# Performance work log

Measured on AMD Instinct MI355X. Metric: run time of the kernel, lower is better.

The kernel has to match this reference:

```python
import jax, jax.numpy as jnp
import numpy as np

B, T, D, K = 16, 4096, 512, 256
ALPHA_MIN = 1e-6


def setup_inputs() -> dict:
    key = jax.random.key(0)
    ks = jax.random.split(key, 5)
    x = jax.random.normal(ks[0], (B, T, D), dtype=jnp.float32)
    # s_imag ~ U(-pi, pi) as in reset_parameters
    s_imag = jax.random.uniform(ks[1], (K,), minval=-np.pi, maxval=np.pi, dtype=jnp.float32)
    # s_real_raw = softplus^{-1}(target_alpha - alpha_min), target_alpha ~ U(0.01, 0.2)
    target_alpha = jax.random.uniform(ks[2], (K,), minval=0.01, maxval=0.2, dtype=jnp.float32)
    y = jnp.clip(target_alpha - ALPHA_MIN, 1e-8, None)
    s_real_raw = jnp.log(jnp.expm1(y))
    # projection weight/bias (spectral norm applied inside reference)
    W = jax.random.normal(ks[3], (K, D), dtype=jnp.float32) / np.sqrt(D)
    b = jnp.zeros((K,), dtype=jnp.float32)
    tau_raw = jnp.zeros((), dtype=jnp.float32)
    return {"x": x, "s_real_raw": s_real_raw, "s_imag": s_imag,
            "tau_raw": tau_raw, "W": W, "b": b}


def _spectral_normalize(W):
    # one power iteration from a fixed random u (mirrors torch spectral_norm buffer,
    # n_power_iterations=1, eps=1e-7); u,v are stop-gradiented like torch buffers.
    eps = 1e-7
    u0 = jax.random.normal(jax.random.key(42), (W.shape[0],), dtype=W.dtype)
    u0 = u0 / jnp.maximum(jnp.linalg.norm(u0), eps)
    v = W.T @ u0
    v = v / jnp.maximum(jnp.linalg.norm(v), eps)
    u = W @ v
    u = u / jnp.maximum(jnp.linalg.norm(u), eps)
    u = jax.lax.stop_gradient(u)
    v = jax.lax.stop_gradient(v)
    sigma = u @ (W @ v)
    return W / sigma


def reference(x, s_real_raw, s_imag, tau_raw, W, b):
    Bx, Tx, Dx = x.shape
    k = s_imag.shape[0]
    tau = jax.nn.softplus(tau_raw) + 1e-3
    alpha0 = (jax.nn.softplus(s_real_raw) + ALPHA_MIN) * tau  # [k]
    omega0 = s_imag * tau                                     # [k]
    # dt is None path: uniform normalized time step
    dt = jnp.asarray(1.0 / max(Tx - 1, 1), dtype=x.dtype)
    rho = jnp.exp(-alpha0 * dt)   # [k], time-invariant since dt is constant
    ct = jnp.cos(omega0 * dt)     # [k]
    st = jnp.sin(omega0 * dt)     # [k]
    # spectral-normalized linear drive u_t = W_sn x_t + b  -> [B,T,k]
    u = jnp.einsum('btd,kd->btk', x, _spectral_normalize(W)) + b

    def step(carry, u_t):
        c, s = carry  # each [B,k]
        c_new = rho * (c * ct - s * st) + u_t
        s_new = rho * (c * st + s * ct)
        return (c_new, s_new), (c_new, s_new)

    z0 = (jnp.zeros((Bx, k), x.dtype), jnp.zeros((Bx, k), x.dtype))
    _, (C, S) = jax.lax.scan(step, z0, jnp.swapaxes(u, 0, 1))  # [T,B,k] each
    C = jnp.swapaxes(C, 0, 1)
    S = jnp.swapaxes(S, 0, 1)
    return jnp.concatenate([C, S], axis=2)  # [B,T,2k]
```

## Files before the change

kernel.cpp:

```cpp
#include <hip/hip_runtime.h>

#define Bsz 16
#define Tsz 4096
#define Dsz 512
#define Ksz 256
#define Msz (Bsz * Tsz)
#define CHUNK 64
#define NCH (Tsz / CHUNK)

typedef __attribute__((ext_vector_type(8))) short short8;
typedef __attribute__((ext_vector_type(4))) float f32x4;

__device__ __forceinline__ unsigned int rotl32(unsigned int x, int d) {
  return (x << d) | (x >> (32 - d));
}

__device__ void threefry_pair(unsigned int c0, unsigned int c1,
                              unsigned int& o0, unsigned int& o1) {
  const unsigned int k0 = 0u, k1 = 42u;
  const unsigned int k2 = k0 ^ k1 ^ 0x1BD11BDAu;
  unsigned int x0 = c0 + k0;
  unsigned int x1 = c1 + k1;
#define TF_ROUND(r) { x0 += x1; x1 = rotl32(x1, (r)); x1 ^= x0; }
  TF_ROUND(13) TF_ROUND(15) TF_ROUND(26) TF_ROUND(6)
  x0 += k1; x1 += k2 + 1u;
  TF_ROUND(17) TF_ROUND(29) TF_ROUND(16) TF_ROUND(24)
  x0 += k2; x1 += k0 + 2u;
  TF_ROUND(13) TF_ROUND(15) TF_ROUND(26) TF_ROUND(6)
  x0 += k0; x1 += k1 + 3u;
  TF_ROUND(17) TF_ROUND(29) TF_ROUND(16) TF_ROUND(24)
  x0 += k1; x1 += k2 + 4u;
  TF_ROUND(13) TF_ROUND(15) TF_ROUND(26) TF_ROUND(6)
  x0 += k2; x1 += k0 + 5u;
#undef TF_ROUND
  o0 = x0; o1 = x1;
}

__device__ float erfinv32(float x) {
  float w = -log1pf(-x * x);
  float p;
  if (w < 5.f) {
    w -= 2.5f;
    p = 2.81022636e-08f;
    p = fmaf(p, w, 3.43273939e-07f);
    p = fmaf(p, w, -3.5233877e-06f);
    p = fmaf(p, w, -4.39150654e-06f);
    p = fmaf(p, w, 0.00021858087f);
    p = fmaf(p, w, -0.00125372503f);
    p = fmaf(p, w, -0.00417768164f);
    p = fmaf(p, w, 0.246640727f);
    p = fmaf(p, w, 1.50140941f);
  } else {
    w = sqrtf(w) - 3.f;
    p = -0.000200214257f;
    p = fmaf(p, w, 0.000100950558f);
    p = fmaf(p, w, 0.00134934322f);
    p = fmaf(p, w, -0.00367342844f);
    p = fmaf(p, w, 0.00573950773f);
    p = fmaf(p, w, -0.0076224613f);
    p = fmaf(p, w, 0.00943887047f);
    p = fmaf(p, w, 1.00167406f);
    p = fmaf(p, w, 2.83297682f);
  }
  return p * x;
}

__device__ float bits_to_normal(unsigned int bits) {
  unsigned int fb = (bits >> 9) | 0x3f800000u;
  float f = __uint_as_float(fb) - 1.0f;
  const float lo = -0.99999994f;
  float u = f * 2.0f + lo;
  u = fmaxf(lo, u);
  return 1.41421356f * erfinv32(u);
}

__device__ float block_sum_512(float v, float* s_red) {
  #pragma unroll
  for (int o = 32; o > 0; o >>= 1) v += __shfl_down(v, o);
  const int lane = threadIdx.x & 63, wid = threadIdx.x >> 6;
  if (lane == 0) s_red[wid] = v;
  __syncthreads();
  float r = 0.f;
  #pragma unroll
  for (int i = 0; i < 8; ++i) r += s_red[i];
  __syncthreads();
  return r;
}

__device__ __forceinline__ unsigned int bf16rne(float f) {
  unsigned int u = __float_as_uint(f);
  return (u + 0x7FFFu + ((u >> 16) & 1u)) >> 16;
}

__global__ __launch_bounds__(512) void prep1_kernel(
    const float* __restrict__ W, float* __restrict__ partial_v) {
  __shared__ float s_u0[Ksz];
  __shared__ float s_red[8];
  const int tid = threadIdx.x;
  if (tid < 128) {
    unsigned int y0, y1;
    threefry_pair((unsigned int)tid, (unsigned int)(tid + 128), y0, y1);
    s_u0[tid] = bits_to_normal(y0);
    s_u0[tid + 128] = bits_to_normal(y1);
  }
  __syncthreads();
  float val = (tid < Ksz) ? s_u0[tid] * s_u0[tid] : 0.f;
  float ss = block_sum_512(val, s_red);
  float inv = 1.f / fmaxf(sqrtf(ss), 1e-7f);

  const int k0 = blockIdx.x * 16;
  float acc = 0.f;
  #pragma unroll
  for (int kk = 0; kk < 16; ++kk)
    acc = fmaf(W[(size_t)(k0 + kk) * Dsz + tid], s_u0[k0 + kk], acc);
  partial_v[blockIdx.x * Dsz + tid] = acc * inv;
}

__global__ __launch_bounds__(512) void prep2_kernel(
    const float* __restrict__ W, const float* __restrict__ partial_v,
    float* __restrict__ wv) {
  __shared__ float s_v[Dsz];
  __shared__ float s_red[8];
  __shared__ float s_p[8];
  const int tid = threadIdx.x;
  float acc = 0.f;
  #pragma unroll
  for (int b = 0; b < 16; ++b) acc += partial_v[b * Dsz + tid];
  float ssv = block_sum_512(acc * acc, s_red);
  float invv = 1.f / fmaxf(sqrtf(ssv), 1e-7f);
  s_v[tid] = acc * invv;
  __syncthreads();

  const int k = blockIdx.x * 4 + (tid >> 7);
  const int sub = tid & 127;
  const float* wr = W + (size_t)k * Dsz;
  float p = 0.f;
  #pragma unroll
  for (int j = sub; j < Dsz; j += 128) p = fmaf(wr[j], s_v[j], p);
  #pragma unroll
  for (int o = 32; o > 0; o >>= 1) p += __shfl_down(p, o);
  const int lane = tid & 63, wid = tid >> 6;
  if (lane == 0) s_p[wid] = p;
  __syncthreads();
  if (tid < 4) wv[blockIdx.x * 4 + tid] = s_p[2 * tid] + s_p[2 * tid + 1];
}

__global__ __launch_bounds__(256) void prep3_kernel(
    const float* __restrict__ s_real_raw, const float* __restrict__ s_imag,
    const float* __restrict__ tau_raw, const float* __restrict__ wv,
    float* __restrict__ consts) {
  __shared__ float s_p[4];
  const int tid = threadIdx.x;
  float v = wv[tid];
  float v2 = v * v;
  #pragma unroll
  for (int o = 32; o > 0; o >>= 1) v2 += __shfl_down(v2, o);
  const int lane = tid & 63, wid = tid >> 6;
  if (lane == 0) s_p[wid] = v2;
  __syncthreads();
  float sswv = s_p[0] + s_p[1] + s_p[2] + s_p[3];
  float sigma = sswv / fmaxf(sqrtf(sswv), 1e-7f);
  if (tid == 0) consts[12 * Ksz] = 1.f / sigma;

  float tr = tau_raw[0];
  float tau = fmaxf(tr, 0.f) + log1pf(expf(-fabsf(tr))) + 1e-3f;
  float srr = s_real_raw[tid];
  float sp = fmaxf(srr, 0.f) + log1pf(expf(-fabsf(srr)));
  float alpha0 = (sp + 1e-6f) * tau;
  float omega0 = s_imag[tid] * tau;
  const float dt = 1.f / 4095.f;
  float ad = alpha0 * dt, an = omega0 * dt;
  consts[tid]            = expf(-ad) * cosf(an);
  consts[Ksz + tid]      = expf(-ad) * sinf(an);
  consts[2 * Ksz + tid]  = expf(-ad * 64.f) * cosf(an * 64.f);
  consts[3 * Ksz + tid]  = expf(-ad * 64.f) * sinf(an * 64.f);
  consts[4 * Ksz + tid]  = expf(-ad * 4.f) * cosf(an * 4.f);
  consts[5 * Ksz + tid]  = expf(-ad * 4.f) * sinf(an * 4.f);
  consts[6 * Ksz + tid]  = expf(-ad * 8.f) * cosf(an * 8.f);
  consts[7 * Ksz + tid]  = expf(-ad * 8.f) * sinf(an * 8.f);
  consts[8 * Ksz + tid]  = expf(-ad * 16.f) * cosf(an * 16.f);
  consts[9 * Ksz + tid]  = expf(-ad * 16.f) * sinf(an * 16.f);
  consts[10 * Ksz + tid] = expf(-ad * 32.f) * cosf(an * 32.f);
  consts[11 * Ksz + tid] = expf(-ad * 32.f) * sinf(an * 32.f);
}

__global__ __launch_bounds__(64) void wpack_kernel(
    const float* __restrict__ W, const float* __restrict__ consts,
    unsigned int* __restrict__ WfH, unsigned int* __restrict__ WfL) {
  const int kb = blockIdx.x >> 4;
  const int nb = blockIdx.x & 15;
  const int lane = threadIdx.x;
  const int lr = lane & 15, lg = lane >> 4;
  const float inv_sigma = consts[12 * Ksz];
  const float* src = W + (size_t)(nb * 16 + lr) * Dsz + kb * 32 + lg * 8;
  float v[8];
  *(float4*)&v[0] = *(const float4*)src;
  *(float4*)&v[4] = *(const float4*)(src + 4);
  unsigned int hh[4], ll[4];
  #pragma unroll
  for (int i = 0; i < 4; ++i) {
    float v0 = v[2 * i] * inv_sigma, v1 = v[2 * i + 1] * inv_sigma;
    unsigned int u0 = __float_as_uint(v0);
    unsigned int u1 = __float_as_uint(v1);
    hh[i] = (u0 >> 16) | (u1 & 0xFFFF0000u);
    float r0 = v0 - __uint_as_float(u0 & 0xFFFF0000u);
    float r1 = v1 - __uint_as_float(u1 & 0xFFFF0000u);
    ll[i] = bf16rne(r0) | (bf16rne(r1) << 16);
  }
  const size_t off = (size_t)blockIdx.x * 256 + lane * 4;
  *(int4*)(WfH + off) = *(int4*)hh;
  *(int4*)(WfL + off) = *(int4*)ll;
}

__global__ __launch_bounds__(512, 2) void gemm_mfma(
    const float* __restrict__ X, const unsigned int* __restrict__ WfH,
    const unsigned int* __restrict__ WfL, const float* __restrict__ bias,
    const float* __restrict__ consts, unsigned short* __restrict__ U,
    float* __restrict__ carry) {
  __shared__ unsigned int ldsA[2][4096];

  const int tid = threadIdx.x;
  const size_t m0 = (size_t)blockIdx.x * 128;

  const int sr = tid >> 2;
  const int sc = (tid & 3) * 8;
  const float* gx = X + (m0 + sr) * Dsz + sc;
  const int swz = (sr & 7) << 4;
  const int aoff_h = sr * 128 + ((sc * 2) ^ swz);
  const int aoff_l = sr * 128 + ((64 + sc * 2) ^ swz);

  const int lane = tid & 63;
  const int wid = tid >> 6;
  const int wm = wid >> 2;
  const int wn = wid & 3;
  const int lr = lane & 15;
  const int lg = lane >> 4;

  float xaA[8], xaB[8];
  #define LOAD_A(dst, kb) do {                             \
    const float* p = gx + (kb) * 32;                       \
    *(float4*)&dst[0] = *(const float4*)p;                 \
    *(float4*)&dst[4] = *(const float4*)(p + 4);           \
  } while (0)

  const char* const wfh = (const char*)WfH + (size_t)wn * 4096 + lane * 16;
  const char* const wfl = (const char*)WfL + (size_t)wn * 4096 + lane * 16;

  short8 bhA[4], blA[4], bhB[4], blB[4];
  #define LOAD_B(bh_, bl_, kb) do {                                          \
    const size_t tb = (size_t)(kb) * 16384;                                  \
    _Pragma("unroll")                                                        \
    for (int f = 0; f < 4; ++f) {                                            \
      bh_[f] = *(const short8*)(wfh + tb + (size_t)f * 1024);                \
      bl_[f] = *(const short8*)(wfl + tb + (size_t)f * 1024);                \
    }                                                                        \
  } while (0)

  #define CONVERT_STORE(xa, buf) do {                                        \
    char* const Ab_ = (char*)ldsA[(buf)];                                    \
    unsigned int hh[4], llw[4];                                              \
    _Pragma("unroll")                                                        \
    for (int i = 0; i < 4; ++i) {                                            \
      float v0 = xa[2 * i], v1 = xa[2 * i + 1];                              \
      unsigned int u0 = __float_as_uint(v0);                                 \
      unsigned int u1 = __float_as_uint(v1);                                 \
      hh[i] = (u0 >> 16) | (u1 & 0xFFFF0000u);                               \
      float r0 = v0 - __uint_as_float(u0 & 0xFFFF0000u);                     \
      float r1 = v1 - __uint_as_float(u1 & 0xFFFF0000u);                     \
      llw[i] = bf16rne(r0) | (bf16rne(r1) << 16);                            \
    }                                                                        \
    *(int4*)(Ab_ + aoff_h) = *(int4*)hh;                                     \
    *(int4*)(Ab_ + aoff_l) = *(int4*)llw;                                    \
  } while (0)

  short8 ah[4], al[4];
  #define DS_READ(buf) do {                                                  \
    const char* const Ab_ = (const char*)ldsA[(buf)];                        \
    _Pragma("unroll")                                                        \
    for (int f = 0; f < 4; ++f) {                                            \
      const int r = wm * 64 + f * 16 + lr;                                   \
      const int sz = (r & 7) << 4;                                           \
      ah[f] = *(const short8*)(Ab_ + r * 128 + ((lg * 16) ^ sz));            \
      al[f] = *(const short8*)(Ab_ + r * 128 + ((64 + lg * 16) ^ sz));       \
    }                                                                        \
  } while (0)

  f32x4 acc[4][4];
  #pragma unroll
  for (int i = 0; i < 4; ++i)
    #pragma unroll
    for (int j = 0; j < 4; ++j) acc[i][j] = (f32x4)(0.f);

  #define MFMA48(bh_, bl_) do {                                              \
    _Pragma("unroll")                                                        \
    for (int mf = 0; mf < 4; ++mf)                                           \
      _Pragma("unroll")                                                      \
      for (int nf = 0; nf < 4; ++nf)                                         \
        acc[mf][nf] = __builtin_amdgcn_mfma_f32_16x16x32_bf16(               \
            ah[mf], bh_[nf], acc[mf][nf], 0, 0, 0);                          \
    _Pragma("unroll")                                                        \
    for (int mf = 0; mf < 4; ++mf)                                           \
      _Pragma("unroll")                                                      \
      for (int nf = 0; nf < 4; ++nf)                                         \
        acc[mf][nf] = __builtin_amdgcn_mfma_f32_16x16x32_bf16(               \
            ah[mf], bl_[nf], acc[mf][nf], 0, 0, 0);                          \
    _Pragma("unroll")                                                        \
    for (int mf = 0; mf < 4; ++mf)                                           \
      _Pragma("unroll")                                                      \
      for (int nf = 0; nf < 4; ++nf)                                         \
        acc[mf][nf] = __builtin_amdgcn_mfma_f32_16x16x32_bf16(               \
            al[mf], bh_[nf], acc[mf][nf], 0, 0, 0);                          \
  } while (0)

  #define SYNC() do {                                                        \
    asm volatile("s_waitcnt lgkmcnt(0)" ::: "memory");                       \
    __builtin_amdgcn_s_barrier();                                            \
    __builtin_amdgcn_sched_barrier(0);                                       \
  } while (0)

  LOAD_A(xaA, 0);
  LOAD_A(xaB, 1);
  LOAD_B(bhA, blA, 0);

  #define BODY(kb, xa, bhC, blC, bhN, blN) do {                              \
    char* const Ab = (char*)ldsA[(kb) & 1]; (void)Ab;                        \
    if ((kb) + 1 < 16) LOAD_B(bhN, blN, (kb) + 1);        \
    CONVERT_STORE(xa, (kb) & 1);                                             \
    if ((kb) + 2 < 16) LOAD_A(xa, (kb) + 2);                   \
    SYNC();                                                                  \
    DS_READ((kb) & 1);                                                       \
    MFMA48(bhC, blC);                                                        \
  } while (0)

  for (int kb = 0; kb < 16; kb += 2) {
    BODY(kb,     xaA, bhA, blA, bhB, blB);
    BODY(kb + 1, xaB, bhB, blB, bhA, blA);
  }
  #undef BODY
  #undef SYNC
  #undef MFMA48
  #undef DS_READ
  #undef CONVERT_STORE
  #undef LOAD_B
  #undef LOAD_A

  #pragma unroll
  for (int nf = 0; nf < 4; ++nf) {
    const int n = wn * 64 + nf * 16 + lr;
    const float bv = bias[n];
    const float ar_ = consts[n],           ai_ = consts[Ksz + n];
    const float p4r = consts[4 * Ksz + n], p4i = consts[5 * Ksz + n];
    const float p8r = consts[6 * Ksz + n], p8i = consts[7 * Ksz + n];
    const float p16r = consts[8 * Ksz + n], p16i = consts[9 * Ksz + n];
    const int e = 3 - lg;
    const float b1r = (e & 1) ? p4r : 1.f, b1i = (e & 1) ? p4i : 0.f;
    const float b2r = (e & 2) ? p8r : 1.f, b2i = (e & 2) ? p8i : 0.f;
    float wr = b1r * b2r - b1i * b2i;
    float wi = b1r * b2i + b1i * b2r;
    float Sr = 0.f, Si = 0.f;
    #pragma unroll
    for (int mf = 3; mf >= 0; --mf) {
      float vr = wr, vi = wi;
      #pragma unroll
      for (int j = 3; j >= 0; --j) {
        const float u = acc[mf][nf][j] + bv;
        U[(m0 + wm * 64 + mf * 16 + lg * 4 + j) * Ksz + n] =
            (unsigned short)bf16rne(u);
        Sr = fmaf(u, vr, Sr);
        Si = fmaf(u, vi, Si);
        if (j) {
          float t_ = vr * ar_ - vi * ai_;
          vi = vr * ai_ + vi * ar_;
          vr = t_;
        }
      }
      if (mf) {
        float t_ = wr * p16r - wi * p16i;
        wi = wr * p16i + wi * p16r;
        wr = t_;
      }
    }
    Sr += __shfl_xor(Sr, 16); Si += __shfl_xor(Si, 16);
    Sr += __shfl_xor(Sr, 32); Si += __shfl_xor(Si, 32);
    if (lg == 0)
      ((float2*)carry)[(size_t)(blockIdx.x * 2 + wm) * Ksz + n] =
          make_float2(Sr, Si);
  }
}

__global__ __launch_bounds__(64) void scan_prefix(
    const float* __restrict__ consts, const float* __restrict__ carry,
    float* __restrict__ prefix) {
  const int k = blockIdx.y * 64 + threadIdx.x;
  const int b = blockIdx.x;
  const float Ar = consts[2 * Ksz + k], Ai = consts[3 * Ksz + k];
  const float2* cp = (const float2*)carry;
  float2* pp = (float2*)prefix;
  float c = 0.f, s = 0.f;
  for (int m = 0; m < NCH; ++m) {
    const size_t idx = (size_t)(b * NCH + m) * Ksz + k;
    pp[idx] = make_float2(c, s);
    float2 L = cp[idx];
    float cn = fmaf(Ar, c, fmaf(-Ai, s, L.x));
    float sn = fmaf(Ai, c, fmaf(Ar, s, L.y));
    c = cn; s = sn;
  }
}

__global__ __launch_bounds__(256) void scan_final(
    const unsigned short* __restrict__ U, const float* __restrict__ consts,
    const float* __restrict__ prefix, float* __restrict__ out) {
  const int k = threadIdx.x;
  const int bm = blockIdx.x;
  const float ar = consts[k], ai = consts[Ksz + k];
  float2 w = ((const float2*)prefix)[(size_t)bm * Ksz + k];
  float c = w.x, s = w.y;
  const unsigned short* up = U + (size_t)bm * (CHUNK * Ksz) + k;
  float* op = out + (size_t)bm * (CHUNK * 2 * Ksz);
  #pragma unroll 4
  for (int t = 0; t < CHUNK; ++t) {
    float u = __uint_as_float((unsigned int)up[(size_t)t * Ksz] << 16);
    float cn = fmaf(ar, c, fmaf(-ai, s, u));
    s = fmaf(ai, c, ar * s);
    c = cn;
    op[(size_t)t * 2 * Ksz + k] = c;
    op[(size_t)t * 2 * Ksz + Ksz + k] = s;
  }
}

extern "C" void kernel_launch(void* const* d_in, const int* in_sizes, int n_in,
                              void* d_out, int out_size, void* d_ws, size_t ws_size,
                              hipStream_t stream) {
  const float* x    = (const float*)d_in[0];
  const float* srr  = (const float*)d_in[1];
  const float* sim  = (const float*)d_in[2];
  const float* traw = (const float*)d_in[3];
  const float* W    = (const float*)d_in[4];
  const float* bias = (const float*)d_in[5];
  float* out = (float*)d_out;

  float* wsf    = (float*)d_ws;
  float* consts = wsf;
  unsigned short* U = (unsigned short*)(wsf + 4096);
  float* carry  = wsf + 4096 + 8388608;
  float* prefix = carry + (size_t)2 * Bsz * NCH * Ksz;
  unsigned int* WfH = (unsigned int*)(prefix + (size_t)2 * Bsz * NCH * Ksz);
  unsigned int* WfL = WfH + 65536;
  float* partial_v  = (float*)(WfL + 65536);
  float* wv         = partial_v + 16 * Dsz;

  prep1_kernel<<<16, 512, 0, stream>>>(W, partial_v);
  prep2_kernel<<<64, 512, 0, stream>>>(W, partial_v, wv);
  prep3_kernel<<<1, 256, 0, stream>>>(srr, sim, traw, wv, consts);
  wpack_kernel<<<256, 64, 0, stream>>>(W, consts, WfH, WfL);
  gemm_mfma<<<Msz / 128, 512, 0, stream>>>(x, WfH, WfL, bias, consts, U, carry);
  scan_prefix<<<dim3(Bsz, Ksz / 64), 64, 0, stream>>>(consts, carry, prefix);
  scan_final<<<Bsz * NCH, Ksz, 0, stream>>>(U, consts, prefix, out);
}
```

Measured before the change: 113.6 us.

## Vectorize scan_final over four channels and use packed bf16 split instructions

scan_final now gives each thread four adjacent channels. It loads U as 64-bit words and writes C and S as float4, and each block covers four chunks, so the grid shrinks to a quarter. This is meant to cut per-element load and store instruction count in the output-bound final pass. Separately, the fp32 to hi/lo bf16 split now uses v_perm and hardware v_cvt_pk_bf16_f32 instead of manual round-to-nearest-even bit arithmetic, which lowers ALU work in the GEMM staging. Risks are fewer blocks and the assumption that the hardware conversion rounds the same way.

```diff
diff --git a/kernel.cpp b/kernel.cpp
--- a/kernel.cpp
+++ b/kernel.cpp
@@ -92,6 +92,18 @@
   return (u + 0x7FFFu + ((u >> 16) & 1u)) >> 16;
 }
 
+__device__ __forceinline__ void split2(float v0, float v1,
+                                       unsigned int& hh, unsigned int& ll) {
+  unsigned int u0 = __float_as_uint(v0);
+  unsigned int u1 = __float_as_uint(v1);
+  hh = __builtin_amdgcn_perm(u1, u0, 0x07060302u);
+  float r0 = v0 - __uint_as_float(u0 & 0xFFFF0000u);
+  float r1 = v1 - __uint_as_float(u1 & 0xFFFF0000u);
+  unsigned int r;
+  asm("v_cvt_pk_bf16_f32 %0, %1, %2" : "=v"(r) : "v"(r0), "v"(r1));
+  ll = r;
+}
+
 __global__ __launch_bounds__(512) void prep1_kernel(
     const float* __restrict__ W, float* __restrict__ partial_v) {
   __shared__ float s_u0[Ksz];
@@ -198,15 +210,8 @@
   *(float4*)&v[4] = *(const float4*)(src + 4);
   unsigned int hh[4], ll[4];
   #pragma unroll
-  for (int i = 0; i < 4; ++i) {
-    float v0 = v[2 * i] * inv_sigma, v1 = v[2 * i + 1] * inv_sigma;
-    unsigned int u0 = __float_as_uint(v0);
-    unsigned int u1 = __float_as_uint(v1);
-    hh[i] = (u0 >> 16) | (u1 & 0xFFFF0000u);
-    float r0 = v0 - __uint_as_float(u0 & 0xFFFF0000u);
-    float r1 = v1 - __uint_as_float(u1 & 0xFFFF0000u);
-    ll[i] = bf16rne(r0) | (bf16rne(r1) << 16);
-  }
+  for (int i = 0; i < 4; ++i)
+    split2(v[2 * i] * inv_sigma, v[2 * i + 1] * inv_sigma, hh[i], ll[i]);
   const size_t off = (size_t)blockIdx.x * 256 + lane * 4;
   *(int4*)(WfH + off) = *(int4*)hh;
   *(int4*)(WfL + off) = *(int4*)ll;
@@ -260,15 +265,8 @@
     char* const Ab_ = (char*)ldsA[(buf)];                                    \
     unsigned int hh[4], llw[4];                                              \
     _Pragma("unroll")                                                        \
-    for (int i = 0; i < 4; ++i) {                                            \
-      float v0 = xa[2 * i], v1 = xa[2 * i + 1];                              \
-      unsigned int u0 = __float_as_uint(v0);                                 \
-      unsigned int u1 = __float_as_uint(v1);                                 \
-      hh[i] = (u0 >> 16) | (u1 & 0xFFFF0000u);                               \
-      float r0 = v0 - __uint_as_float(u0 & 0xFFFF0000u);                     \
-      float r1 = v1 - __uint_as_float(u1 & 0xFFFF0000u);                     \
-      llw[i] = bf16rne(r0) | (bf16rne(r1) << 16);                            \
-    }                                                                        \
+    for (int i = 0; i < 4; ++i)                                              \
+      split2(xa[2 * i], xa[2 * i + 1], hh[i], llw[i]);                       \
     *(int4*)(Ab_ + aoff_h) = *(int4*)hh;                                     \
     *(int4*)(Ab_ + aoff_l) = *(int4*)llw;                                    \
   } while (0)
@@ -323,7 +321,6 @@
   LOAD_B(bhA, blA, 0);
 
   #define BODY(kb, xa, bhC, blC, bhN, blN) do {                              \
-    char* const Ab = (char*)ldsA[(kb) & 1]; (void)Ab;                        \
     if ((kb) + 1 < 16) LOAD_B(bhN, blN, (kb) + 1);        \
     CONVERT_STORE(xa, (kb) & 1);                                             \
     if ((kb) + 2 < 16) LOAD_A(xa, (kb) + 2);                   \
@@ -410,21 +407,31 @@
 __global__ __launch_bounds__(256) void scan_final(
     const unsigned short* __restrict__ U, const float* __restrict__ consts,
     const float* __restrict__ prefix, float* __restrict__ out) {
-  const int k = threadIdx.x;
-  const int bm = blockIdx.x;
-  const float ar = consts[k], ai = consts[Ksz + k];
-  float2 w = ((const float2*)prefix)[(size_t)bm * Ksz + k];
-  float c = w.x, s = w.y;
-  const unsigned short* up = U + (size_t)bm * (CHUNK * Ksz) + k;
-  float* op = out + (size_t)bm * (CHUNK * 2 * Ksz);
-  #pragma unroll 4
+  const int tid = threadIdx.x;
+  const int bm = blockIdx.x * 4 + (tid >> 6);
+  const int k0 = (tid & 63) * 4;
+  float ar[4], ai[4], c[4], s[4];
+  #pragma unroll
+  for (int j = 0; j < 4; ++j) {
+    ar[j] = consts[k0 + j];
+    ai[j] = consts[Ksz + k0 + j];
+    float2 w = ((const float2*)prefix)[(size_t)bm * Ksz + k0 + j];
+    c[j] = w.x; s[j] = w.y;
+  }
+  const unsigned short* up = U + (size_t)bm * (CHUNK * Ksz) + k0;
+  float* op = out + (size_t)bm * (CHUNK * 2 * Ksz) + k0;
   for (int t = 0; t < CHUNK; ++t) {
-    float u = __uint_as_float((unsigned int)up[(size_t)t * Ksz] << 16);
-    float cn = fmaf(ar, c, fmaf(-ai, s, u));
-    s = fmaf(ai, c, ar * s);
-    c = cn;
-    op[(size_t)t * 2 * Ksz + k] = c;
-    op[(size_t)t * 2 * Ksz + Ksz + k] = s;
+    unsigned long long uv = *(const unsigned long long*)(up + (size_t)t * Ksz);
+    #pragma unroll
+    for (int j = 0; j < 4; ++j) {
+      float u = __uint_as_float(((unsigned int)(uv >> (16 * j))) << 16);
+      float cn = fmaf(ar[j], c[j], fmaf(-ai[j], s[j], u));
+      s[j] = fmaf(ai[j], c[j], ar[j] * s[j]);
+      c[j] = cn;
+    }
+    *(float4*)(op + (size_t)t * 2 * Ksz) = make_float4(c[0], c[1], c[2], c[3]);
+    *(float4*)(op + (size_t)t * 2 * Ksz + Ksz) =
+        make_float4(s[0], s[1], s[2], s[3]);
   }
 }
 
@@ -455,5 +462,5 @@
   wpack_kernel<<<256, 64, 0, stream>>>(W, consts, WfH, WfL);
   gemm_mfma<<<Msz / 128, 512, 0, stream>>>(x, WfH, WfL, bias, consts, U, carry);
   scan_prefix<<<dim3(Bsz, Ksz / 64), 64, 0, stream>>>(consts, carry, prefix);
-  scan_final<<<Bsz * NCH, Ksz, 0, stream>>>(U, consts, prefix, out);
-}
+  scan_final<<<Bsz * NCH / 4, 256, 0, stream>>>(U, consts, prefix, out);
+}
```

Result: no change. 113.9 us (+0.2%).
